# Kernel optimization log

Hardware: AMD Instinct MI355X
Metric: run time of the kernel (lower is better)

## Reference

```python
import math
import jax, jax.numpy as jnp
import numpy as np

B, T, H = 4096, 49, 512

def setup_inputs() -> dict:
    key = jax.random.key(0)
    ks = jax.random.split(key, 13)
    sc = 1.0 / math.sqrt(H)
    return {
        "v": jax.random.normal(ks[0], (B, T, H), dtype=jnp.float32),
        "h": jax.random.normal(ks[1], (B, H), dtype=jnp.float32),
        "s": jax.random.normal(ks[2], (B, H), dtype=jnp.float32),
        "W_h": jax.random.normal(ks[3], (H, H), dtype=jnp.float32) * sc,
        "b_h": jax.random.normal(ks[4], (H,), dtype=jnp.float32) * sc,
        "W_v": jax.random.normal(ks[5], (H, H), dtype=jnp.float32) * sc,
        "b_v": jax.random.normal(ks[6], (H,), dtype=jnp.float32) * sc,
        "w_z": jax.random.normal(ks[7], (H,), dtype=jnp.float32) * sc,
        "b_z": jax.random.normal(ks[8], (), dtype=jnp.float32) * sc,
        "W_s": jax.random.normal(ks[9], (H, H), dtype=jnp.float32) * sc,
        "b_s": jax.random.normal(ks[10], (H,), dtype=jnp.float32) * sc,
        "w_beta": jax.random.normal(ks[11], (H,), dtype=jnp.float32) * sc,
        "b_beta": jax.random.normal(ks[12], (), dtype=jnp.float32) * sc,
    }

def reference(v, h, s, W_h, b_h, W_v, b_v, w_z, b_z, W_s, b_s, w_beta, b_beta):
    # eval mode: dropout is identity
    h_proj = h @ W_h + b_h                                  # [B, H]
    v_proj = jnp.einsum('bth,hk->btk', v, W_v) + b_v        # [B, T, H]
    z = jnp.tanh(h_proj[:, None, :] + v_proj)               # [B, T, H]
    z = jnp.einsum('bth,h->bt', z, w_z) + b_z               # [B, T]
    beta = jnp.tanh((s @ W_s + b_s + h_proj) * math.sqrt(0.5))  # [B, H]
    beta = (beta @ w_beta + b_beta)[:, None]                # [B, 1]
    a = jax.nn.softmax(jnp.concatenate([z, beta], axis=1), axis=1)  # [B, T+1]
    v_ext = jnp.concatenate([v, s[:, None, :]], axis=1)     # [B, T+1, H]
    c = jnp.einsum('bt,bth->bh', a, v_ext)                  # [B, H]
    return c
```

## Files before the change

kernel.cpp:

```cpp
#include <hip/hip_runtime.h>
#include <stdint.h>

#define B_ 4096
#define T_ 49
#define H_ 512
#define BT_ (B_*T_)
#define BB 16

typedef __bf16 bf16x8 __attribute__((ext_vector_type(8)));
typedef float  f32x4  __attribute__((ext_vector_type(4)));
typedef unsigned short ushort_;

__device__ __forceinline__ ushort_ f2bf(float f){
  unsigned int u = __float_as_uint(f);
  u += 0x7fffu + ((u >> 16) & 1u);
  return (ushort_)(u >> 16);
}

__device__ __forceinline__ float fast_tanh(float x){
  float e = __expf(2.0f * x);
  return 1.0f - 2.0f * __builtin_amdgcn_rcpf(e + 1.0f);
}

__global__ __launch_bounds__(256) void k_pack(const float* __restrict__ Wv,
                                              ushort_* __restrict__ bpack){
  int idx = blockIdx.x * 256 + threadIdx.x;
  int lane = idx & 63;
  int gt   = (idx >> 6) & 31;
  int kk   = idx >> 11;
  int col  = gt*16 + (lane & 15);
  int k0   = kk*32 + (lane >> 4)*8;
  ushort4 lo, hi;
  lo.x = f2bf(Wv[(k0+0)*H_ + col]);
  lo.y = f2bf(Wv[(k0+1)*H_ + col]);
  lo.z = f2bf(Wv[(k0+2)*H_ + col]);
  lo.w = f2bf(Wv[(k0+3)*H_ + col]);
  hi.x = f2bf(Wv[(k0+4)*H_ + col]);
  hi.y = f2bf(Wv[(k0+5)*H_ + col]);
  hi.z = f2bf(Wv[(k0+6)*H_ + col]);
  hi.w = f2bf(Wv[(k0+7)*H_ + col]);
  ushort4* dst = (ushort4*)bpack;
  dst[idx*2]   = lo;
  dst[idx*2+1] = hi;
}

__global__ __launch_bounds__(512) void k_proj(
    const float* __restrict__ h, const float* __restrict__ s,
    const float* __restrict__ Wh, const float* __restrict__ bh,
    const float* __restrict__ Ws, const float* __restrict__ bs,
    const float* __restrict__ bv, const float* __restrict__ wbeta,
    const float* __restrict__ bbeta_p,
    float* __restrict__ hpb, float* __restrict__ beta)
{
  __shared__ float hs[H_*BB];
  __shared__ float ssm[H_*BB];
  __shared__ float part[BB][8];
  const int tid = threadIdx.x;
  const int b0 = blockIdx.x * BB;

  for(int idx = tid; idx < H_*BB; idx += 512){
    int bb2 = idx & (BB-1);
    int j   = idx >> 4;
    hs[idx]  = h[(size_t)(b0+bb2)*H_ + j];
    ssm[idx] = s[(size_t)(b0+bb2)*H_ + j];
  }
  __syncthreads();

  const int k = tid;
  float ah[BB], as_[BB];
  #pragma unroll
  for(int i=0;i<BB;i++){ ah[i]=0.f; as_[i]=0.f; }

  #pragma unroll 4
  for(int j=0;j<H_;j++){
    float whv = Wh[j*H_ + k];
    float wsv = Ws[j*H_ + k];
    #pragma unroll
    for(int i=0;i<BB;i++){
      ah[i]  = fmaf(hs[j*BB+i],  whv, ah[i]);
      as_[i] = fmaf(ssm[j*BB+i], wsv, as_[i]);
    }
  }

  const float bhk = bh[k], bsk = bs[k], bvk = bv[k], wbk = wbeta[k];
  const float bbv = bbeta_p[0];
  const int lane = tid & 63, wid = tid >> 6;

  #pragma unroll
  for(int i=0;i<BB;i++){
    float hp = ah[i] + bhk;
    hpb[(size_t)(b0+i)*H_ + k] = hp + bvk;
    float bt = fast_tanh((as_[i] + bsk + hp) * 0.70710678118654752f);
    float c = bt * wbk;
    #pragma unroll
    for(int m=32;m>=1;m>>=1) c += __shfl_xor(c, m);
    if(lane == 0) part[i][wid] = c;
  }
  __syncthreads();
  if(tid < BB){
    float acc = bbv;
    #pragma unroll
    for(int wq=0; wq<8; wq++) acc += part[tid][wq];
    beta[b0+tid] = acc;
  }
}

__global__ __launch_bounds__(256, 2) void k_fused(
    const float* __restrict__ v, const ushort_* __restrict__ bpack,
    const float* __restrict__ hpb, const float* __restrict__ wz,
    const float* __restrict__ bz_p, const float* __restrict__ beta,
    const float* __restrict__ s, float* __restrict__ out)
{
  __shared__ __align__(16) ushort_ Av[49*512];
  __shared__ float zw[4][64];
  __shared__ float a_s[64];
  const int tid = threadIdx.x;
  const int w = tid >> 6, lane = tid & 63;
  const int l15 = lane & 15, l4 = lane >> 4;
  const int b = blockIdx.x;

  const f32x4* __restrict__ vsrc = (const f32x4*)(v + (size_t)b * T_ * H_);
  const bf16x8* __restrict__ bp = (const bf16x8*)bpack;
  const int bbase = w*512 + lane;

  const int srow = tid >> 4, c4 = tid & 15;
  const int slot = ((c4 >> 1) ^ (srow & 7));
  const int wsub = ((c4 & 1) << 3);

  {
    f32x4 nf0 = __builtin_nontemporal_load(vsrc + (srow      )*128 + c4);
    f32x4 nf1 = __builtin_nontemporal_load(vsrc + (srow + 16 )*128 + c4);
    f32x4 nf2 = __builtin_nontemporal_load(vsrc + (srow + 32 )*128 + c4);
    f32x4 nf3;
    if(tid < 16) nf3 = __builtin_nontemporal_load(vsrc + 48*128 + c4);
    ushort4 u;
    u.x=f2bf(nf0[0]); u.y=f2bf(nf0[1]); u.z=f2bf(nf0[2]); u.w=f2bf(nf0[3]);
    *(ushort4*)((char*)Av + (srow   )*1024 + (slot<<4) + wsub) = u;
    u.x=f2bf(nf1[0]); u.y=f2bf(nf1[1]); u.z=f2bf(nf1[2]); u.w=f2bf(nf1[3]);
    *(ushort4*)((char*)Av + (srow+16)*1024 + (slot<<4) + wsub) = u;
    u.x=f2bf(nf2[0]); u.y=f2bf(nf2[1]); u.z=f2bf(nf2[2]); u.w=f2bf(nf2[3]);
    *(ushort4*)((char*)Av + (srow+32)*1024 + (slot<<4) + wsub) = u;
    if(tid < 16){
      u.x=f2bf(nf3[0]); u.y=f2bf(nf3[1]); u.z=f2bf(nf3[2]); u.w=f2bf(nf3[3]);
      *(ushort4*)((char*)Av + 48*1024 + (slot<<4) + wsub) = u;
    }
  }

  f32x4 acc[4][8];
  #pragma unroll
  for(int mi=0;mi<4;mi++)
    #pragma unroll
    for(int ni=0;ni<8;ni++) acc[mi][ni] = (f32x4){0.f,0.f,0.f,0.f};

  __syncthreads();

  #pragma unroll 1
  for(int c=0;c<8;c++){
    bf16x8 b0[8], b1[8];
    #pragma unroll
    for(int ni=0;ni<8;ni++) b0[ni] = bp[(2*c  )*2048 + bbase + ni*64];
    #pragma unroll
    for(int ni=0;ni<8;ni++) b1[ni] = bp[(2*c+1)*2048 + bbase + ni*64];
    f32x4 nf0, nf1, nf2, nf3;
    if(c < 7){
      nf0 = __builtin_nontemporal_load(vsrc + (srow      )*128 + (c+1)*16 + c4);
      nf1 = __builtin_nontemporal_load(vsrc + (srow + 16 )*128 + (c+1)*16 + c4);
      nf2 = __builtin_nontemporal_load(vsrc + (srow + 32 )*128 + (c+1)*16 + c4);
      if(tid < 16) nf3 = __builtin_nontemporal_load(vsrc + 48*128 + (c+1)*16 + c4);
    }
    bf16x8 af[4];
    #pragma unroll
    for(int mi=0;mi<4;mi++){
      int row = (mi < 3) ? (mi*16 + l15) : 48;
      int g   = ((2*c)*4 + l4) ^ (row & 7);
      af[mi] = *(const bf16x8*)((const char*)Av + row*1024 + (g<<4));
    }
    #pragma unroll
    for(int mi=0;mi<4;mi++)
      #pragma unroll
      for(int ni=0;ni<8;ni++)
        acc[mi][ni] = __builtin_amdgcn_mfma_f32_16x16x32_bf16(af[mi], b0[ni], acc[mi][ni], 0,0,0);
    #pragma unroll
    for(int mi=0;mi<4;mi++){
      int row = (mi < 3) ? (mi*16 + l15) : 48;
      int g   = ((2*c+1)*4 + l4) ^ (row & 7);
      af[mi] = *(const bf16x8*)((const char*)Av + row*1024 + (g<<4));
    }
    #pragma unroll
    for(int mi=0;mi<4;mi++)
      #pragma unroll
      for(int ni=0;ni<8;ni++)
        acc[mi][ni] = __builtin_amdgcn_mfma_f32_16x16x32_bf16(af[mi], b1[ni], acc[mi][ni], 0,0,0);
    if(c < 7){
      const int cb = (c+1)*128;
      ushort4 u;
      u.x=f2bf(nf0[0]); u.y=f2bf(nf0[1]); u.z=f2bf(nf0[2]); u.w=f2bf(nf0[3]);
      *(ushort4*)((char*)Av + (srow   )*1024 + cb + (slot<<4) + wsub) = u;
      u.x=f2bf(nf1[0]); u.y=f2bf(nf1[1]); u.z=f2bf(nf1[2]); u.w=f2bf(nf1[3]);
      *(ushort4*)((char*)Av + (srow+16)*1024 + cb + (slot<<4) + wsub) = u;
      u.x=f2bf(nf2[0]); u.y=f2bf(nf2[1]); u.z=f2bf(nf2[2]); u.w=f2bf(nf2[3]);
      *(ushort4*)((char*)Av + (srow+32)*1024 + cb + (slot<<4) + wsub) = u;
      if(tid < 16){
        u.x=f2bf(nf3[0]); u.y=f2bf(nf3[1]); u.z=f2bf(nf3[2]); u.w=f2bf(nf3[3]);
        *(ushort4*)((char*)Av + 48*1024 + cb + (slot<<4) + wsub) = u;
      }
    }
    __syncthreads();
  }

  float wzv[8], hp0[8];
  #pragma unroll
  for(int ni=0;ni<8;ni++){
    int col = w*128 + ni*16 + l15;
    wzv[ni] = wz[col];
    hp0[ni] = hpb[(size_t)b*H_ + col];
  }
  float zp[16];
  #pragma unroll
  for(int mi=0;mi<4;mi++){
    #pragma unroll
    for(int r=0;r<4;r++){
      float az = 0.f;
      #pragma unroll
      for(int ni=0;ni<8;ni++)
        az = fmaf(fast_tanh(acc[mi][ni][r] + hp0[ni]), wzv[ni], az);
      zp[mi*4+r] = az;
    }
  }
  #pragma unroll
  for(int i=0;i<16;i++){
    zp[i] += __shfl_xor(zp[i], 1);
    zp[i] += __shfl_xor(zp[i], 2);
    zp[i] += __shfl_xor(zp[i], 4);
    zp[i] += __shfl_xor(zp[i], 8);
  }
  if(l15 == 0){
    #pragma unroll
    for(int mi=0;mi<4;mi++)
      #pragma unroll
      for(int r=0;r<4;r++)
        zw[w][mi*16 + l4*4 + r] = zp[mi*4+r];
  }
  __syncthreads();

  if(tid < 64){
    float zv;
    if(tid < T_)       zv = zw[0][tid] + zw[1][tid] + zw[2][tid] + zw[3][tid] + bz_p[0];
    else if(tid == T_) zv = beta[b];
    else               zv = -3.0e38f;
    float m = zv;
    #pragma unroll
    for(int off=32;off>=1;off>>=1) m = fmaxf(m, __shfl_xor(m, off));
    float e = (tid <= T_) ? __expf(zv - m) : 0.f;
    float ssum = e;
    #pragma unroll
    for(int off=32;off>=1;off>>=1) ssum += __shfl_xor(ssum, off);
    a_s[tid] = e * __builtin_amdgcn_rcpf(ssum);
  }
  __syncthreads();

  const int n0 = tid * 2;
  float ax = 0.f, ay = 0.f;
  #pragma unroll 7
  for(int t=0;t<T_;t++){
    float at = a_s[t];
    unsigned int u = *(const unsigned int*)((const char*)Av + t*1024
                       + ((((n0>>3) ^ (t&7)))<<4) + ((n0&7)<<1));
    float x = __uint_as_float((u & 0xFFFFu) << 16);
    float y = __uint_as_float(u & 0xFFFF0000u);
    ax = fmaf(at, x, ax);
    ay = fmaf(at, y, ay);
  }
  float a49 = a_s[T_];
  float2 sv = ((const float2*)(s + (size_t)b*H_))[tid];
  ax = fmaf(a49, sv.x, ax);
  ay = fmaf(a49, sv.y, ay);
  float2 res; res.x = ax; res.y = ay;
  ((float2*)(out + (size_t)b*H_))[tid] = res;
}

extern "C" void kernel_launch(void* const* d_in, const int* in_sizes, int n_in,
                              void* d_out, int out_size, void* d_ws, size_t ws_size,
                              hipStream_t stream)
{
  const float* v   = (const float*)d_in[0];
  const float* h   = (const float*)d_in[1];
  const float* s   = (const float*)d_in[2];
  const float* Wh  = (const float*)d_in[3];
  const float* bh  = (const float*)d_in[4];
  const float* Wv  = (const float*)d_in[5];
  const float* bv  = (const float*)d_in[6];
  const float* wz  = (const float*)d_in[7];
  const float* bz  = (const float*)d_in[8];
  const float* Ws  = (const float*)d_in[9];
  const float* bs  = (const float*)d_in[10];
  const float* wb  = (const float*)d_in[11];
  const float* bbet= (const float*)d_in[12];
  float* out = (float*)d_out;

  float* hpb  = (float*)d_ws;
  float* beta = hpb + (size_t)B_*H_;
  ushort_* bpack = (ushort_*)(beta + B_);

  k_pack <<<128, 256, 0, stream>>>(Wv, bpack);
  k_proj <<<B_/BB, 512, 0, stream>>>(h, s, Wh, bh, Ws, bs, bv, wb, bbet, hpb, beta);
  k_fused<<<B_, 256, 0, stream>>>(v, bpack, hpb, wz, bz, beta, s, out);
}
```

Before: 266.4 us.

## Compute h and s projections with bf16 MFMA using packed weights

Replaces the FP32 scalar-FMA projection kernel with one that converts h and s rows to bf16 in shared memory in MFMA fragment order. It computes h@W_h and s@W_s with 16x16x32 bf16 MFMA instructions. W_h and W_s are pre-packed into bf16 fragment layout by reusing the existing pack kernel, which adds two extra launches. The aim is to cut the FP32 ALU cost of the projections, at the price of bf16 rounding on the h_proj and beta inputs.

```diff
diff --git a/kernel.cpp b/kernel.cpp
--- a/kernel.cpp
+++ b/kernel.cpp
@@ -22,8 +22,8 @@
   return 1.0f - 2.0f * __builtin_amdgcn_rcpf(e + 1.0f);
 }
 
-__global__ __launch_bounds__(256) void k_pack(const float* __restrict__ Wv,
-                                              ushort_* __restrict__ bpack){
+__global__ __launch_bounds__(256) void k_pack(const float* __restrict__ W,
+                                              ushort_* __restrict__ pack){
   int idx = blockIdx.x * 256 + threadIdx.x;
   int lane = idx & 63;
   int gt   = (idx >> 6) & 31;
@@ -31,78 +31,105 @@
   int col  = gt*16 + (lane & 15);
   int k0   = kk*32 + (lane >> 4)*8;
   ushort4 lo, hi;
-  lo.x = f2bf(Wv[(k0+0)*H_ + col]);
-  lo.y = f2bf(Wv[(k0+1)*H_ + col]);
-  lo.z = f2bf(Wv[(k0+2)*H_ + col]);
-  lo.w = f2bf(Wv[(k0+3)*H_ + col]);
-  hi.x = f2bf(Wv[(k0+4)*H_ + col]);
-  hi.y = f2bf(Wv[(k0+5)*H_ + col]);
-  hi.z = f2bf(Wv[(k0+6)*H_ + col]);
-  hi.w = f2bf(Wv[(k0+7)*H_ + col]);
-  ushort4* dst = (ushort4*)bpack;
+  lo.x = f2bf(W[(k0+0)*H_ + col]);
+  lo.y = f2bf(W[(k0+1)*H_ + col]);
+  lo.z = f2bf(W[(k0+2)*H_ + col]);
+  lo.w = f2bf(W[(k0+3)*H_ + col]);
+  hi.x = f2bf(W[(k0+4)*H_ + col]);
+  hi.y = f2bf(W[(k0+5)*H_ + col]);
+  hi.z = f2bf(W[(k0+6)*H_ + col]);
+  hi.w = f2bf(W[(k0+7)*H_ + col]);
+  ushort4* dst = (ushort4*)pack;
   dst[idx*2]   = lo;
   dst[idx*2+1] = hi;
 }
 
-__global__ __launch_bounds__(512) void k_proj(
+__global__ __launch_bounds__(256) void k_proj2(
     const float* __restrict__ h, const float* __restrict__ s,
-    const float* __restrict__ Wh, const float* __restrict__ bh,
-    const float* __restrict__ Ws, const float* __restrict__ bs,
+    const ushort_* __restrict__ whp, const ushort_* __restrict__ wsp,
+    const float* __restrict__ bh, const float* __restrict__ bs,
     const float* __restrict__ bv, const float* __restrict__ wbeta,
     const float* __restrict__ bbeta_p,
     float* __restrict__ hpb, float* __restrict__ beta)
 {
-  __shared__ float hs[H_*BB];
-  __shared__ float ssm[H_*BB];
-  __shared__ float part[BB][8];
+  __shared__ __align__(16) ushort_ hl[16*H_];
+  __shared__ __align__(16) ushort_ sl[16*H_];
+  __shared__ float zwp[4][16];
   const int tid = threadIdx.x;
-  const int b0 = blockIdx.x * BB;
-
-  for(int idx = tid; idx < H_*BB; idx += 512){
-    int bb2 = idx & (BB-1);
-    int j   = idx >> 4;
-    hs[idx]  = h[(size_t)(b0+bb2)*H_ + j];
-    ssm[idx] = s[(size_t)(b0+bb2)*H_ + j];
-  }
-  __syncthreads();
-
-  const int k = tid;
-  float ah[BB], as_[BB];
-  #pragma unroll
-  for(int i=0;i<BB;i++){ ah[i]=0.f; as_[i]=0.f; }
-
-  #pragma unroll 4
-  for(int j=0;j<H_;j++){
-    float whv = Wh[j*H_ + k];
-    float wsv = Ws[j*H_ + k];
-    #pragma unroll
-    for(int i=0;i<BB;i++){
-      ah[i]  = fmaf(hs[j*BB+i],  whv, ah[i]);
-      as_[i] = fmaf(ssm[j*BB+i], wsv, as_[i]);
-    }
-  }
-
-  const float bhk = bh[k], bsk = bs[k], bvk = bv[k], wbk = wbeta[k];
-  const float bbv = bbeta_p[0];
-  const int lane = tid & 63, wid = tid >> 6;
-
-  #pragma unroll
-  for(int i=0;i<BB;i++){
-    float hp = ah[i] + bhk;
-    hpb[(size_t)(b0+i)*H_ + k] = hp + bvk;
-    float bt = fast_tanh((as_[i] + bsk + hp) * 0.70710678118654752f);
-    float c = bt * wbk;
-    #pragma unroll
-    for(int m=32;m>=1;m>>=1) c += __shfl_xor(c, m);
-    if(lane == 0) part[i][wid] = c;
-  }
-  __syncthreads();
-  if(tid < BB){
-    float acc = bbv;
-    #pragma unroll
-    for(int wq=0; wq<8; wq++) acc += part[tid][wq];
-    beta[b0+tid] = acc;
-  }
+  const int w = tid >> 6, lane = tid & 63;
+  const int l15 = lane & 15, l4 = lane >> 4;
+  const int b0 = blockIdx.x * 16;
+
+  {
+    const int r = tid >> 4;
+    const float4* hsrc = (const float4*)(h + (size_t)(b0+r)*H_);
+    const float4* ssrc = (const float4*)(s + (size_t)(b0+r)*H_);
+    #pragma unroll
+    for(int p=0;p<8;p++){
+      int q  = (tid & 15) + p*16;
+      int k0 = q*4;
+      float4 fh = hsrc[q];
+      float4 fs = ssrc[q];
+      int idx = (k0>>5)*512 + ((((k0&31)>>3)<<4) + r)*8 + (k0&7);
+      ushort4 uh; uh.x=f2bf(fh.x); uh.y=f2bf(fh.y); uh.z=f2bf(fh.z); uh.w=f2bf(fh.w);
+      ushort4 us; us.x=f2bf(fs.x); us.y=f2bf(fs.y); us.z=f2bf(fs.z); us.w=f2bf(fs.w);
+      *(ushort4*)&hl[idx] = uh;
+      *(ushort4*)&sl[idx] = us;
+    }
+  }
+  __syncthreads();
+
+  const bf16x8* __restrict__ bph = (const bf16x8*)whp;
+  const bf16x8* __restrict__ bps = (const bf16x8*)wsp;
+  const int bbase = w*512 + lane;
+
+  f32x4 acch[8], accs[8];
+  #pragma unroll
+  for(int ni=0;ni<8;ni++){ acch[ni]=(f32x4){0,0,0,0}; accs[ni]=(f32x4){0,0,0,0}; }
+
+  #pragma unroll 2
+  for(int kk=0;kk<16;kk++){
+    bf16x8 ah = *(const bf16x8*)&hl[kk*512 + lane*8];
+    bf16x8 as2 = *(const bf16x8*)&sl[kk*512 + lane*8];
+    #pragma unroll
+    for(int ni=0;ni<8;ni++){
+      acch[ni] = __builtin_amdgcn_mfma_f32_16x16x32_bf16(ah,  bph[kk*2048 + bbase + ni*64], acch[ni], 0,0,0);
+      accs[ni] = __builtin_amdgcn_mfma_f32_16x16x32_bf16(as2, bps[kk*2048 + bbase + ni*64], accs[ni], 0,0,0);
+    }
+  }
+
+  float bhv[8], bsv[8], bvv[8], wbv[8];
+  #pragma unroll
+  for(int ni=0;ni<8;ni++){
+    int col = w*128 + ni*16 + l15;
+    bhv[ni] = bh[col]; bsv[ni] = bs[col]; bvv[ni] = bv[col]; wbv[ni] = wbeta[col];
+  }
+  float btsum[4];
+  #pragma unroll
+  for(int rr=0;rr<4;rr++){
+    int row = l4*4 + rr;
+    float bsum = 0.f;
+    #pragma unroll
+    for(int ni=0;ni<8;ni++){
+      int col = w*128 + ni*16 + l15;
+      float hp = acch[ni][rr] + bhv[ni];
+      hpb[(size_t)(b0+row)*H_ + col] = hp + bvv[ni];
+      float bt = fast_tanh((accs[ni][rr] + bsv[ni] + hp) * 0.70710678118654752f);
+      bsum = fmaf(bt, wbv[ni], bsum);
+    }
+    btsum[rr] = bsum;
+  }
+  #pragma unroll
+  for(int rr=0;rr<4;rr++){
+    btsum[rr] += __shfl_xor(btsum[rr], 1);
+    btsum[rr] += __shfl_xor(btsum[rr], 2);
+    btsum[rr] += __shfl_xor(btsum[rr], 4);
+    btsum[rr] += __shfl_xor(btsum[rr], 8);
+    if(l15 == 0) zwp[w][l4*4+rr] = btsum[rr];
+  }
+  __syncthreads();
+  if(tid < 16)
+    beta[b0+tid] = zwp[0][tid] + zwp[1][tid] + zwp[2][tid] + zwp[3][tid] + bbeta_p[0];
 }
 
 __global__ __launch_bounds__(256, 2) void k_fused(
@@ -301,8 +328,12 @@
   float* hpb  = (float*)d_ws;
   float* beta = hpb + (size_t)B_*H_;
   ushort_* bpack = (ushort_*)(beta + B_);
+  ushort_* whp   = bpack + (size_t)H_*H_;
+  ushort_* wsp   = whp   + (size_t)H_*H_;
 
   k_pack <<<128, 256, 0, stream>>>(Wv, bpack);
-  k_proj <<<B_/BB, 512, 0, stream>>>(h, s, Wh, bh, Ws, bs, bv, wb, bbet, hpb, beta);
+  k_pack <<<128, 256, 0, stream>>>(Wh, whp);
+  k_pack <<<128, 256, 0, stream>>>(Ws, wsp);
+  k_proj2<<<B_/16, 256, 0, stream>>>(h, s, whp, wsp, bh, bs, bv, wb, bbet, hpb, beta);
   k_fused<<<B_, 256, 0, stream>>>(v, bpack, hpb, wz, bz, beta, s, out);
 }
```

Result: faster. 217.2 us (-18.5%).
